# Performance work log

Measured on AMD Instinct MI355X. Metric: run time of the kernel, lower is better.

The kernel has to match this reference:

```python
import jax, jax.numpy as jnp
import numpy as np
import math

DIM_IN = 2
DIM_HIDDEN = 64
DIM_OUT = 16
NUM_LAYERS = 5  # num_layers-1 = 4 hidden SirenLayers per subnet + 1 last layer
W0 = 30.0
W0_INITIAL = 30.0
S0 = 0.0
C = 6.0
N_POINTS = 262144


def wire(w0, s0, z):
    # sin(w0*z) * exp(-(s0*z)^2)
    return jnp.sin(w0 * z) * jnp.exp(-jnp.square(s0 * z))


def setup_inputs() -> dict:
    key = jax.random.key(0)
    ks = jax.random.split(key, 8)
    # NOTE: source passes is_first=False for every layer, so init bound is
    # sqrt(c/dim_in)/layer_w0 for ALL layers (including the first).
    std0 = math.sqrt(C / DIM_IN) / W0_INITIAL
    stdh = math.sqrt(C / DIM_HIDDEN) / W0
    stdl = math.sqrt(C / DIM_HIDDEN) / W0
    u = lambda k, shape, s: jax.random.uniform(k, shape, jnp.float32, -s, s)
    nmid = NUM_LAYERS - 2  # hidden->hidden layers per subnet (3)
    return {
        "x": jax.random.uniform(ks[0], (N_POINTS, DIM_IN), jnp.float32),
        "W0m": u(ks[1], (DIM_OUT, DIM_HIDDEN, DIM_IN), std0),
        "b0": u(ks[2], (DIM_OUT, DIM_HIDDEN), std0),
        "Wm": u(ks[3], (nmid, DIM_OUT, DIM_HIDDEN, DIM_HIDDEN), stdh),
        "bm": u(ks[4], (nmid, DIM_OUT, DIM_HIDDEN), stdh),
        "Wl": u(ks[5], (DIM_OUT, DIM_HIDDEN), stdl),
        "bl": u(ks[6], (DIM_OUT,), stdl),
    }


def reference(x, W0m, b0, Wm, bm, Wl, bl):
    # First layer of each subnet (uses w0_initial): [N,D] x [O,H,D] -> [N,O,H]
    h = wire(W0_INITIAL, S0, jnp.einsum("nd,ohd->noh", x, W0m) + b0)
    # Middle hidden layers (w0), scanned over the fixed layer stack.
    def body(h, wb):
        W, b = wb
        h = wire(W0, S0, jnp.einsum("noh,ogh->nog", h, W) + b)
        return h, None
    h, _ = jax.lax.scan(body, h, (Wm, bm))
    # Last layer per subnet: dim 1 output each, is_last -> +0.5, no activation.
    out = jnp.einsum("noh,oh->no", h, Wl) + bl + 0.5  # [N, dim_out]
    return out
```

## Files before the change

### kernel.cpp

```cpp
#include <hip/hip_runtime.h>

typedef short bf16x8 __attribute__((ext_vector_type(8)));
typedef float f32x16 __attribute__((ext_vector_type(16)));

#define NBGROUPS 96
#define NTILES   8192
#define SCALE 4.7746482927568601f

union Frag  { bf16x8 v; unsigned u[4]; uint4 q; };
union AccLd { float4 f4[4]; f32x16 v; };

__device__ __forceinline__ unsigned pk_bf16(float lo, float hi) {
    unsigned r;
    asm("v_cvt_pk_bf16_f32 %0, %1, %2" : "=v"(r) : "v"(lo), "v"(hi));
    return r;
}
__device__ __forceinline__ float lo_f(unsigned w) { return __uint_as_float(w << 16); }
__device__ __forceinline__ float hi_f(unsigned w) { return __uint_as_float(w & 0xffff0000u); }

__device__ __forceinline__ float sin_rev(float z) {
    float v  = z - rintf(z);
    float v2 = v * v;
    float p  = 32.765379f;
    p = fmaf(p, v2, -74.468884f);
    p = fmaf(p, v2,  81.365064f);
    p = fmaf(p, v2, -41.331084f);
    p = fmaf(p, v2,   6.2830526f);
    return p * v;
}

__device__ __forceinline__ void init_acc(f32x16* acc, const float4* ldsBias, int Lb, int hi) {
#pragma unroll
    for (int tg = 0; tg < 2; ++tg) {
        AccLd a;
        const float4* base = &ldsBias[((Lb*2+tg)*2 + hi)*4];
#pragma unroll
        for (int q = 0; q < 4; ++q) a.f4[q] = base[q];
        acc[tg] = a.v;
    }
}

__device__ __forceinline__ void transitionHL(const f32x16* acc, Frag* Bhi, Frag* Blo) {
#pragma unroll
    for (int tg = 0; tg < 2; ++tg) {
        float sv[16];
#pragma unroll
        for (int r = 0; r < 16; ++r) sv[r] = sin_rev(acc[tg][r]);
#pragma unroll
        for (int s = 0; s < 2; ++s)
#pragma unroll
            for (int wi = 0; wi < 4; ++wi) {
                float a = sv[s*8 + 2*wi], b = sv[s*8 + 2*wi + 1];
                unsigned ph = pk_bf16(a, b);
                Bhi[tg*2+s].u[wi] = ph;
                Blo[tg*2+s].u[wi] = pk_bf16(a - lo_f(ph), b - hi_f(ph));
            }
    }
}
__device__ __forceinline__ void transitionH(const f32x16* acc, Frag* Bhi) {
#pragma unroll
    for (int tg = 0; tg < 2; ++tg) {
        float sv[16];
#pragma unroll
        for (int r = 0; r < 16; ++r) sv[r] = sin_rev(acc[tg][r]);
#pragma unroll
        for (int s = 0; s < 2; ++s)
#pragma unroll
            for (int wi = 0; wi < 4; ++wi)
                Bhi[tg*2+s].u[wi] = pk_bf16(sv[s*8 + 2*wi], sv[s*8 + 2*wi + 1]);
    }
}

__global__ __launch_bounds__(256, 3)
void siren_kernel(const float* __restrict__ x, const float* __restrict__ W0m,
                  const float* __restrict__ b0, const float* __restrict__ Wm,
                  const float* __restrict__ bm, const float* __restrict__ Wl,
                  const float* __restrict__ bl, float* __restrict__ out)
{
    __shared__ uint4  ldsAhi[3*2*4*64];
    __shared__ uint4  ldsAlo[3*2*4*64];
    __shared__ float4 ldsBias[4*2*2*4];

    const int tid  = threadIdx.x;
    const int pg   = blockIdx.x;
    const int o    = blockIdx.y;
    const int lane = tid & 63;
    const int wv   = tid >> 6;
    const int col  = lane & 31;
    const int hi   = lane >> 5;

    for (int idx = tid; idx < 3*2*4*64; idx += 256) {
        int l2  = idx & 63;
        int fi  = idx >> 6;
        int c   = fi & 3;
        int tg  = (fi >> 2) & 1;
        int L   = fi >> 3;
        int hi2 = l2 >> 5;
        int g   = tg*32 + (l2 & 31);
        int th  = c >> 1, s = c & 1;
        const float2* Wrow2 = (const float2*)(Wm + (((size_t)(L*16 + o)*64 + g)*64));
        uint4 whi, wlo;
        unsigned* uh = (unsigned*)&whi;
        unsigned* ul = (unsigned*)&wlo;
#pragma unroll
        for (int wi = 0; wi < 4; ++wi) {
            int h = th*32 + s*16 + 8*(wi>>1) + 2*(wi&1) + 4*hi2;
            float2 wp = Wrow2[h >> 1];
            float a = SCALE*wp.x, b = SCALE*wp.y;
            unsigned ph = pk_bf16(a, b);
            uh[wi] = ph;
            ul[wi] = pk_bf16(a - lo_f(ph), b - hi_f(ph));
        }
        ldsAhi[idx] = whi;
        ldsAlo[idx] = wlo;
    }
    if (tid < 64) {
        int q   = tid & 3;
        int hi2 = (tid >> 2) & 1;
        int tg  = (tid >> 3) & 1;
        int Lb  = tid >> 4;
        int h0  = tg*32 + 8*q + 4*hi2;
        const float* bsrc = (Lb < 3) ? (bm + (Lb*16 + o)*64) : (b0 + o*64);
        ldsBias[tid] = make_float4(SCALE*bsrc[h0], SCALE*bsrc[h0+1],
                                   SCALE*bsrc[h0+2], SCALE*bsrc[h0+3]);
    }

    Frag L1A[2];
#pragma unroll
    for (int tg = 0; tg < 2; ++tg) {
        int g = tg*32 + col;
        float2 wp = ((const float2*)W0m)[o*64 + g];
        float s0 = SCALE*wp.x, s1 = SCALE*wp.y;
        unsigned u0 = pk_bf16(s0, s0), u1 = pk_bf16(s1, s1);
        float l0 = s0 - lo_f(u0), l1 = s1 - lo_f(u1);
        L1A[tg].u[0] = hi ? 0u : u0;
        L1A[tg].u[1] = hi ? 0u : u1;
        L1A[tg].u[2] = hi ? 0u : pk_bf16(l0, l0);
        L1A[tg].u[3] = hi ? 0u : pk_bf16(l1, l1);
    }
    Frag WlA[4];
#pragma unroll
    for (int c = 0; c < 4; ++c) { WlA[c].u[0]=0u; WlA[c].u[1]=0u; WlA[c].u[2]=0u; WlA[c].u[3]=0u; }
    if (col == 0) {
        const float2* Wl2 = (const float2*)(Wl + o*64);
#pragma unroll
        for (int c = 0; c < 4; ++c) {
            int tg = c >> 1, s = c & 1;
#pragma unroll
            for (int wi = 0; wi < 4; ++wi) {
                int h = tg*32 + s*16 + 8*(wi>>1) + 2*(wi&1) + 4*hi;
                float2 wp = Wl2[h >> 1];
                WlA[c].u[wi] = pk_bf16(wp.x, wp.y);
            }
        }
    }
    const float blv = bl[o] + 0.5f;

    __syncthreads();

    const int tend = ((pg + 1) * NTILES) / NBGROUPS;
    for (int t = (pg * NTILES) / NBGROUPS + wv; t < tend; t += 4) {
        const int pp = t*32 + col;

        float2 xv = ((const float2*)x)[pp];
        unsigned ux = pk_bf16(xv.x, xv.y);
        float x0h = lo_f(ux), x1h = hi_f(ux);
        unsigned w0 = pk_bf16(x0h, xv.x - x0h);
        unsigned w1 = pk_bf16(x1h, xv.y - x1h);
        Frag B1;
        B1.u[0] = hi ? 0u : w0;
        B1.u[1] = hi ? 0u : w1;
        B1.u[2] = hi ? 0u : w0;
        B1.u[3] = hi ? 0u : w1;

        f32x16 acc[2];
        init_acc(acc, ldsBias, 3, hi);
        acc[0] = __builtin_amdgcn_mfma_f32_32x32x16_bf16(L1A[0].v, B1.v, acc[0], 0, 0, 0);
        acc[1] = __builtin_amdgcn_mfma_f32_32x32x16_bf16(L1A[1].v, B1.v, acc[1], 0, 0, 0);

        Frag Bhi[4], Blo[4];
        transitionHL(acc, Bhi, Blo);

#pragma unroll
        for (int L = 0; L < 3; ++L) {
            init_acc(acc, ldsBias, L, hi);
#pragma unroll
            for (int c = 0; c < 4; ++c) {
                Frag Ah0, Ah1, Al0, Al1;
                Ah0.q = ldsAhi[((L*2+0)*4+c)*64 + lane];
                Ah1.q = ldsAhi[((L*2+1)*4+c)*64 + lane];
                Al0.q = ldsAlo[((L*2+0)*4+c)*64 + lane];
                Al1.q = ldsAlo[((L*2+1)*4+c)*64 + lane];
                acc[0] = __builtin_amdgcn_mfma_f32_32x32x16_bf16(Ah0.v, Bhi[c].v, acc[0], 0, 0, 0);
                acc[1] = __builtin_amdgcn_mfma_f32_32x32x16_bf16(Ah1.v, Bhi[c].v, acc[1], 0, 0, 0);
                acc[0] = __builtin_amdgcn_mfma_f32_32x32x16_bf16(Ah0.v, Blo[c].v, acc[0], 0, 0, 0);
                acc[1] = __builtin_amdgcn_mfma_f32_32x32x16_bf16(Ah1.v, Blo[c].v, acc[1], 0, 0, 0);
                acc[0] = __builtin_amdgcn_mfma_f32_32x32x16_bf16(Al0.v, Bhi[c].v, acc[0], 0, 0, 0);
                acc[1] = __builtin_amdgcn_mfma_f32_32x32x16_bf16(Al1.v, Bhi[c].v, acc[1], 0, 0, 0);
            }
            if (L < 2) transitionHL(acc, Bhi, Blo);
        }

        transitionH(acc, Bhi);
        f32x16 facc;
#pragma unroll
        for (int i = 0; i < 16; ++i) facc[i] = 0.f;
        facc[0] = blv;
#pragma unroll
        for (int c = 0; c < 4; ++c)
            facc = __builtin_amdgcn_mfma_f32_32x32x16_bf16(WlA[c].v, Bhi[c].v, facc, 0, 0, 0);
        if (lane < 32) out[(size_t)pp*16 + o] = facc[0];
    }
}

extern "C" void kernel_launch(void* const* d_in, const int* in_sizes, int n_in,
                              void* d_out, int out_size, void* d_ws, size_t ws_size,
                              hipStream_t stream) {
    (void)in_sizes; (void)n_in; (void)out_size; (void)d_ws; (void)ws_size;
    siren_kernel<<<dim3(NBGROUPS, 16), dim3(256), 0, stream>>>(
        (const float*)d_in[0], (const float*)d_in[1], (const float*)d_in[2],
        (const float*)d_in[3], (const float*)d_in[4], (const float*)d_in[5],
        (const float*)d_in[6], (float*)d_out);
}
```

Measured before the change: 397.5 us.

## Rewrite SIREN kernel with 16x16x32 MFMA, dual tiles, packed sin, reduced split precision

The kernel is rebuilt around 16x16x32 bf16 MFMAs, with each wave processing two 16-point tiles at once so that every LDS weight fragment is reused across both. The sine polynomial is computed on packed float pairs. The last hidden layer drops its low-order bf16 correction terms, and the final linear layer becomes a VALU FMA reduction with shuffles instead of a mostly-zero MFMA. Block size goes to 512 threads with a fixed 16-iteration loop and 64 point groups. The intent is less wasted MFMA work and better weight reuse, at the cost of some accuracy in the last layer and a fixed tiling that assumes N is 262144.

```diff
diff --git a/kernel.cpp b/kernel.cpp
--- a/kernel.cpp
+++ b/kernel.cpp
@@ -1,15 +1,17 @@
 #include <hip/hip_runtime.h>
 
-typedef short bf16x8 __attribute__((ext_vector_type(8)));
-typedef float f32x16 __attribute__((ext_vector_type(16)));
-
-#define NBGROUPS 96
-#define NTILES   8192
+typedef float    f32x4 __attribute__((ext_vector_type(4)));
+typedef float    f32x2 __attribute__((ext_vector_type(2)));
+typedef unsigned u32x4 __attribute__((ext_vector_type(4)));
+
+#define NBGROUPS 64
 #define SCALE 4.7746482927568601f
 
-union Frag  { bf16x8 v; unsigned u[4]; uint4 q; };
-union AccLd { float4 f4[4]; f32x16 v; };
-
+union Frag { unsigned u[4]; u32x4 q; };
+
+__device__ __forceinline__ void mfma16(f32x4& d, u32x4 a, u32x4 b) {
+    asm("v_mfma_f32_16x16x32_bf16 %0, %1, %2, %0" : "+v"(d) : "v"(a), "v"(b));
+}
 __device__ __forceinline__ unsigned pk_bf16(float lo, float hi) {
     unsigned r;
     asm("v_cvt_pk_bf16_f32 %0, %1, %2" : "=v"(r) : "v"(lo), "v"(hi));
@@ -18,198 +20,254 @@
 __device__ __forceinline__ float lo_f(unsigned w) { return __uint_as_float(w << 16); }
 __device__ __forceinline__ float hi_f(unsigned w) { return __uint_as_float(w & 0xffff0000u); }
 
-__device__ __forceinline__ float sin_rev(float z) {
-    float v  = z - rintf(z);
-    float v2 = v * v;
-    float p  = 32.765379f;
-    p = fmaf(p, v2, -74.468884f);
-    p = fmaf(p, v2,  81.365064f);
-    p = fmaf(p, v2, -41.331084f);
-    p = fmaf(p, v2,   6.2830526f);
+__device__ __forceinline__ f32x2 sin2(f32x2 z) {
+    f32x2 r  = { rintf(z.x), rintf(z.y) };
+    f32x2 v  = z - r;
+    f32x2 v2 = v * v;
+    f32x2 p  = { 32.765379f, 32.765379f };
+    p = __builtin_elementwise_fma(p, v2, (f32x2){-74.468884f, -74.468884f});
+    p = __builtin_elementwise_fma(p, v2, (f32x2){ 81.365064f,  81.365064f});
+    p = __builtin_elementwise_fma(p, v2, (f32x2){-41.331084f, -41.331084f});
+    p = __builtin_elementwise_fma(p, v2, (f32x2){  6.2830526f,  6.2830526f});
     return p * v;
 }
 
-__device__ __forceinline__ void init_acc(f32x16* acc, const float4* ldsBias, int Lb, int hi) {
-#pragma unroll
-    for (int tg = 0; tg < 2; ++tg) {
-        AccLd a;
-        const float4* base = &ldsBias[((Lb*2+tg)*2 + hi)*4];
-#pragma unroll
-        for (int q = 0; q < 4; ++q) a.f4[q] = base[q];
-        acc[tg] = a.v;
-    }
-}
-
-__device__ __forceinline__ void transitionHL(const f32x16* acc, Frag* Bhi, Frag* Blo) {
-#pragma unroll
-    for (int tg = 0; tg < 2; ++tg) {
-        float sv[16];
-#pragma unroll
-        for (int r = 0; r < 16; ++r) sv[r] = sin_rev(acc[tg][r]);
-#pragma unroll
-        for (int s = 0; s < 2; ++s)
-#pragma unroll
-            for (int wi = 0; wi < 4; ++wi) {
-                float a = sv[s*8 + 2*wi], b = sv[s*8 + 2*wi + 1];
-                unsigned ph = pk_bf16(a, b);
-                Bhi[tg*2+s].u[wi] = ph;
-                Blo[tg*2+s].u[wi] = pk_bf16(a - lo_f(ph), b - hi_f(ph));
+__device__ __forceinline__ f32x4 bias_c(const f32x4* ldsBias, int Lb, int t, int g2) {
+    return ldsBias[(Lb*4 + t)*4 + g2];
+}
+
+__device__ __forceinline__ void transHL(const f32x4* acc, Frag* Bhi, Frag* Blo) {
+#pragma unroll
+    for (int m = 0; m < 2; ++m)
+#pragma unroll
+        for (int s = 0; s < 2; ++s) {
+            const int t = 2*m + s;
+#pragma unroll
+            for (int jp = 0; jp < 2; ++jp) {
+                f32x2 z = { acc[t][2*jp], acc[t][2*jp+1] };
+                f32x2 sv = sin2(z);
+                unsigned ph = pk_bf16(sv.x, sv.y);
+                f32x2 hf = { lo_f(ph), hi_f(ph) };
+                f32x2 d  = sv - hf;
+                Bhi[m].u[2*s+jp] = ph;
+                Blo[m].u[2*s+jp] = pk_bf16(d.x, d.y);
             }
-    }
-}
-__device__ __forceinline__ void transitionH(const f32x16* acc, Frag* Bhi) {
-#pragma unroll
-    for (int tg = 0; tg < 2; ++tg) {
-        float sv[16];
-#pragma unroll
-        for (int r = 0; r < 16; ++r) sv[r] = sin_rev(acc[tg][r]);
-#pragma unroll
-        for (int s = 0; s < 2; ++s)
-#pragma unroll
-            for (int wi = 0; wi < 4; ++wi)
-                Bhi[tg*2+s].u[wi] = pk_bf16(sv[s*8 + 2*wi], sv[s*8 + 2*wi + 1]);
-    }
-}
-
-__global__ __launch_bounds__(256, 3)
+        }
+}
+__device__ __forceinline__ void transH(const f32x4* acc, Frag* Bhi) {
+#pragma unroll
+    for (int m = 0; m < 2; ++m)
+#pragma unroll
+        for (int s = 0; s < 2; ++s) {
+            const int t = 2*m + s;
+#pragma unroll
+            for (int jp = 0; jp < 2; ++jp) {
+                f32x2 z = { acc[t][2*jp], acc[t][2*jp+1] };
+                f32x2 sv = sin2(z);
+                Bhi[m].u[2*s+jp] = pk_bf16(sv.x, sv.y);
+            }
+        }
+}
+
+__device__ __forceinline__ void layerHL(f32x4* accA, f32x4* accB,
+        const Frag* BhiA, const Frag* BloA, const Frag* BhiB, const Frag* BloB,
+        const u32x4* ldsAhi, const u32x4* ldsAlo, int L, int lane) {
+#pragma unroll
+    for (int m = 0; m < 2; ++m)
+#pragma unroll
+        for (int t = 0; t < 4; ++t) {
+            u32x4 Ah = ldsAhi[((L*4+t)*2+m)*64 + lane];
+            u32x4 Al = ldsAlo[((L*4+t)*2+m)*64 + lane];
+            mfma16(accA[t], Ah, BhiA[m].q);
+            mfma16(accB[t], Ah, BhiB[m].q);
+            mfma16(accA[t], Ah, BloA[m].q);
+            mfma16(accB[t], Ah, BloB[m].q);
+            mfma16(accA[t], Al, BhiA[m].q);
+            mfma16(accB[t], Al, BhiB[m].q);
+        }
+}
+__device__ __forceinline__ void layerH(f32x4* accA, f32x4* accB,
+        const Frag* BhiA, const Frag* BhiB,
+        const u32x4* ldsAhi, int L, int lane) {
+#pragma unroll
+    for (int m = 0; m < 2; ++m)
+#pragma unroll
+        for (int t = 0; t < 4; ++t) {
+            u32x4 Ah = ldsAhi[((L*4+t)*2+m)*64 + lane];
+            mfma16(accA[t], Ah, BhiA[m].q);
+            mfma16(accB[t], Ah, BhiB[m].q);
+        }
+}
+
+__global__ __launch_bounds__(512, 4)
 void siren_kernel(const float* __restrict__ x, const float* __restrict__ W0m,
                   const float* __restrict__ b0, const float* __restrict__ Wm,
                   const float* __restrict__ bm, const float* __restrict__ Wl,
                   const float* __restrict__ bl, float* __restrict__ out)
 {
-    __shared__ uint4  ldsAhi[3*2*4*64];
-    __shared__ uint4  ldsAlo[3*2*4*64];
-    __shared__ float4 ldsBias[4*2*2*4];
+    __shared__ u32x4 ldsAhi[3*4*2*64];
+    __shared__ u32x4 ldsAlo[2*4*2*64];
+    __shared__ f32x4 ldsBias[4*4*4];
+    __shared__ float ldsWl[4][16];
 
     const int tid  = threadIdx.x;
     const int pg   = blockIdx.x;
     const int o    = blockIdx.y;
     const int lane = tid & 63;
     const int wv   = tid >> 6;
-    const int col  = lane & 31;
-    const int hi   = lane >> 5;
-
-    for (int idx = tid; idx < 3*2*4*64; idx += 256) {
-        int l2  = idx & 63;
-        int fi  = idx >> 6;
-        int c   = fi & 3;
-        int tg  = (fi >> 2) & 1;
-        int L   = fi >> 3;
-        int hi2 = l2 >> 5;
-        int g   = tg*32 + (l2 & 31);
-        int th  = c >> 1, s = c & 1;
+    const int pl   = lane & 15;
+    const int g2   = lane >> 4;
+
+    for (int idx = tid; idx < 3*4*2*64; idx += 512) {
+        int l2 = idx & 63;
+        int fi = idx >> 6;
+        int m  = fi & 1;
+        int t  = (fi >> 1) & 3;
+        int L  = fi >> 3;
+        int g  = 16*t + (l2 & 15);
+        int gg = l2 >> 4;
         const float2* Wrow2 = (const float2*)(Wm + (((size_t)(L*16 + o)*64 + g)*64));
-        uint4 whi, wlo;
+        u32x4 whi, wlo;
         unsigned* uh = (unsigned*)&whi;
         unsigned* ul = (unsigned*)&wlo;
 #pragma unroll
-        for (int wi = 0; wi < 4; ++wi) {
-            int h = th*32 + s*16 + 8*(wi>>1) + 2*(wi&1) + 4*hi2;
-            float2 wp = Wrow2[h >> 1];
+        for (int w = 0; w < 4; ++w) {
+            int s  = w >> 1, jp = (w & 1) * 2;
+            int k  = 32*m + 16*s + 4*gg + jp;
+            float2 wp = Wrow2[k >> 1];
             float a = SCALE*wp.x, b = SCALE*wp.y;
             unsigned ph = pk_bf16(a, b);
-            uh[wi] = ph;
-            ul[wi] = pk_bf16(a - lo_f(ph), b - hi_f(ph));
+            uh[w] = ph;
+            ul[w] = pk_bf16(a - lo_f(ph), b - hi_f(ph));
         }
         ldsAhi[idx] = whi;
-        ldsAlo[idx] = wlo;
+        if (idx < 2*4*2*64) ldsAlo[idx] = wlo;
     }
     if (tid < 64) {
-        int q   = tid & 3;
-        int hi2 = (tid >> 2) & 1;
-        int tg  = (tid >> 3) & 1;
-        int Lb  = tid >> 4;
-        int h0  = tg*32 + 8*q + 4*hi2;
+        int gg = tid & 3;
+        int t  = (tid >> 2) & 3;
+        int Lb = tid >> 4;
+        int h0 = 16*t + 4*gg;
         const float* bsrc = (Lb < 3) ? (bm + (Lb*16 + o)*64) : (b0 + o*64);
-        ldsBias[tid] = make_float4(SCALE*bsrc[h0], SCALE*bsrc[h0+1],
-                                   SCALE*bsrc[h0+2], SCALE*bsrc[h0+3]);
-    }
-
-    Frag L1A[2];
-#pragma unroll
-    for (int tg = 0; tg < 2; ++tg) {
-        int g = tg*32 + col;
+        ldsBias[tid] = (f32x4){SCALE*bsrc[h0], SCALE*bsrc[h0+1],
+                               SCALE*bsrc[h0+2], SCALE*bsrc[h0+3]};
+    }
+    if (tid >= 64 && tid < 128) {
+        int t2  = tid - 64;
+        int gg  = t2 >> 4;
+        int idx = t2 & 15;
+        int t   = idx >> 2;
+        int j   = idx & 3;
+        ldsWl[gg][idx] = Wl[o*64 + 16*t + 4*gg + j];
+    }
+
+    Frag L1A[4];
+#pragma unroll
+    for (int t = 0; t < 4; ++t) {
+        int g = 16*t + pl;
         float2 wp = ((const float2*)W0m)[o*64 + g];
         float s0 = SCALE*wp.x, s1 = SCALE*wp.y;
-        unsigned u0 = pk_bf16(s0, s0), u1 = pk_bf16(s1, s1);
-        float l0 = s0 - lo_f(u0), l1 = s1 - lo_f(u1);
-        L1A[tg].u[0] = hi ? 0u : u0;
-        L1A[tg].u[1] = hi ? 0u : u1;
-        L1A[tg].u[2] = hi ? 0u : pk_bf16(l0, l0);
-        L1A[tg].u[3] = hi ? 0u : pk_bf16(l1, l1);
-    }
-    Frag WlA[4];
-#pragma unroll
-    for (int c = 0; c < 4; ++c) { WlA[c].u[0]=0u; WlA[c].u[1]=0u; WlA[c].u[2]=0u; WlA[c].u[3]=0u; }
-    if (col == 0) {
-        const float2* Wl2 = (const float2*)(Wl + o*64);
-#pragma unroll
-        for (int c = 0; c < 4; ++c) {
-            int tg = c >> 1, s = c & 1;
-#pragma unroll
-            for (int wi = 0; wi < 4; ++wi) {
-                int h = tg*32 + s*16 + 8*(wi>>1) + 2*(wi&1) + 4*hi;
-                float2 wp = Wl2[h >> 1];
-                WlA[c].u[wi] = pk_bf16(wp.x, wp.y);
+        unsigned u0 = pk_bf16(s0, s0);
+        float w0h = lo_f(u0), w0l = s0 - w0h;
+        unsigned u1 = pk_bf16(s1, s1);
+        float w1h = lo_f(u1), w1l = s1 - w1h;
+        bool zz = (g2 != 0);
+        L1A[t].u[0] = zz ? 0u : u0;
+        L1A[t].u[1] = zz ? 0u : pk_bf16(w0l, w1h);
+        L1A[t].u[2] = zz ? 0u : pk_bf16(w1h, w1l);
+        L1A[t].u[3] = 0u;
+    }
+    const float blv = bl[o] + 0.5f;
+
+    __syncthreads();
+
+#pragma unroll 1
+    for (int it = 0; it < 16; ++it) {
+        const int t32 = pg*128 + it*8 + wv;
+        const int pb  = t32*32;
+
+        float2 xa = ((const float2*)x)[pb + pl];
+        float2 xb = ((const float2*)x)[pb + 16 + pl];
+        Frag B1a, B1b;
+        {
+            unsigned u0 = pk_bf16(xa.x, xa.x);
+            float x0h = lo_f(u0), x0l = xa.x - x0h;
+            unsigned u1 = pk_bf16(xa.y, xa.y);
+            float x1h = lo_f(u1), x1l = xa.y - x1h;
+            B1a.u[0] = pk_bf16(x0h, x0l);
+            B1a.u[1] = pk_bf16(x0h, x1h);
+            B1a.u[2] = pk_bf16(x1l, x1h);
+            B1a.u[3] = 0u;
+            u0 = pk_bf16(xb.x, xb.x); x0h = lo_f(u0); x0l = xb.x - x0h;
+            u1 = pk_bf16(xb.y, xb.y); x1h = lo_f(u1); x1l = xb.y - x1h;
+            B1b.u[0] = pk_bf16(x0h, x0l);
+            B1b.u[1] = pk_bf16(x0h, x1h);
+            B1b.u[2] = pk_bf16(x1l, x1h);
+            B1b.u[3] = 0u;
+        }
+
+        f32x4 accA[4], accB[4];
+#pragma unroll
+        for (int t = 0; t < 4; ++t) {
+            accA[t] = bias_c(ldsBias, 3, t, g2);
+            accB[t] = bias_c(ldsBias, 3, t, g2);
+        }
+#pragma unroll
+        for (int t = 0; t < 4; ++t) mfma16(accA[t], L1A[t].q, B1a.q);
+#pragma unroll
+        for (int t = 0; t < 4; ++t) mfma16(accB[t], L1A[t].q, B1b.q);
+
+        Frag BhiA[2], BloA[2], BhiB[2], BloB[2];
+        transHL(accA, BhiA, BloA);
+        transHL(accB, BhiB, BloB);
+
+#pragma unroll
+        for (int t = 0; t < 4; ++t) {
+            accA[t] = bias_c(ldsBias, 0, t, g2);
+            accB[t] = bias_c(ldsBias, 0, t, g2);
+        }
+        layerHL(accA, accB, BhiA, BloA, BhiB, BloB, ldsAhi, ldsAlo, 0, lane);
+        transHL(accA, BhiA, BloA);
+        transHL(accB, BhiB, BloB);
+
+#pragma unroll
+        for (int t = 0; t < 4; ++t) {
+            accA[t] = bias_c(ldsBias, 1, t, g2);
+            accB[t] = bias_c(ldsBias, 1, t, g2);
+        }
+        layerHL(accA, accB, BhiA, BloA, BhiB, BloB, ldsAhi, ldsAlo, 1, lane);
+        transH(accA, BhiA);
+        transH(accB, BhiB);
+
+#pragma unroll
+        for (int t = 0; t < 4; ++t) {
+            accA[t] = bias_c(ldsBias, 2, t, g2);
+            accB[t] = bias_c(ldsBias, 2, t, g2);
+        }
+        layerH(accA, accB, BhiA, BhiB, ldsAhi, 2, lane);
+
+        const f32x2* wl2 = (const f32x2*)&ldsWl[g2][0];
+        f32x2 sa = {0.f, 0.f}, sb = {0.f, 0.f};
+#pragma unroll
+        for (int t = 0; t < 4; ++t)
+#pragma unroll
+            for (int jp = 0; jp < 2; ++jp) {
+                f32x2 w = wl2[t*2 + jp];
+                f32x2 za = { accA[t][2*jp], accA[t][2*jp+1] };
+                f32x2 zb = { accB[t][2*jp], accB[t][2*jp+1] };
+                sa = __builtin_elementwise_fma(sin2(za), w, sa);
+                sb = __builtin_elementwise_fma(sin2(zb), w, sb);
             }
-        }
-    }
-    const float blv = bl[o] + 0.5f;
-
-    __syncthreads();
-
-    const int tend = ((pg + 1) * NTILES) / NBGROUPS;
-    for (int t = (pg * NTILES) / NBGROUPS + wv; t < tend; t += 4) {
-        const int pp = t*32 + col;
-
-        float2 xv = ((const float2*)x)[pp];
-        unsigned ux = pk_bf16(xv.x, xv.y);
-        float x0h = lo_f(ux), x1h = hi_f(ux);
-        unsigned w0 = pk_bf16(x0h, xv.x - x0h);
-        unsigned w1 = pk_bf16(x1h, xv.y - x1h);
-        Frag B1;
-        B1.u[0] = hi ? 0u : w0;
-        B1.u[1] = hi ? 0u : w1;
-        B1.u[2] = hi ? 0u : w0;
-        B1.u[3] = hi ? 0u : w1;
-
-        f32x16 acc[2];
-        init_acc(acc, ldsBias, 3, hi);
-        acc[0] = __builtin_amdgcn_mfma_f32_32x32x16_bf16(L1A[0].v, B1.v, acc[0], 0, 0, 0);
-        acc[1] = __builtin_amdgcn_mfma_f32_32x32x16_bf16(L1A[1].v, B1.v, acc[1], 0, 0, 0);
-
-        Frag Bhi[4], Blo[4];
-        transitionHL(acc, Bhi, Blo);
-
-#pragma unroll
-        for (int L = 0; L < 3; ++L) {
-            init_acc(acc, ldsBias, L, hi);
-#pragma unroll
-            for (int c = 0; c < 4; ++c) {
-                Frag Ah0, Ah1, Al0, Al1;
-                Ah0.q = ldsAhi[((L*2+0)*4+c)*64 + lane];
-                Ah1.q = ldsAhi[((L*2+1)*4+c)*64 + lane];
-                Al0.q = ldsAlo[((L*2+0)*4+c)*64 + lane];
-                Al1.q = ldsAlo[((L*2+1)*4+c)*64 + lane];
-                acc[0] = __builtin_amdgcn_mfma_f32_32x32x16_bf16(Ah0.v, Bhi[c].v, acc[0], 0, 0, 0);
-                acc[1] = __builtin_amdgcn_mfma_f32_32x32x16_bf16(Ah1.v, Bhi[c].v, acc[1], 0, 0, 0);
-                acc[0] = __builtin_amdgcn_mfma_f32_32x32x16_bf16(Ah0.v, Blo[c].v, acc[0], 0, 0, 0);
-                acc[1] = __builtin_amdgcn_mfma_f32_32x32x16_bf16(Ah1.v, Blo[c].v, acc[1], 0, 0, 0);
-                acc[0] = __builtin_amdgcn_mfma_f32_32x32x16_bf16(Al0.v, Bhi[c].v, acc[0], 0, 0, 0);
-                acc[1] = __builtin_amdgcn_mfma_f32_32x32x16_bf16(Al1.v, Bhi[c].v, acc[1], 0, 0, 0);
-            }
-            if (L < 2) transitionHL(acc, Bhi, Blo);
-        }
-
-        transitionH(acc, Bhi);
-        f32x16 facc;
-#pragma unroll
-        for (int i = 0; i < 16; ++i) facc[i] = 0.f;
-        facc[0] = blv;
-#pragma unroll
-        for (int c = 0; c < 4; ++c)
-            facc = __builtin_amdgcn_mfma_f32_32x32x16_bf16(WlA[c].v, Bhi[c].v, facc, 0, 0, 0);
-        if (lane < 32) out[(size_t)pp*16 + o] = facc[0];
+        float suma = sa.x + sa.y;
+        float sumb = sb.x + sb.y;
+        suma += __shfl_xor(suma, 16);
+        suma += __shfl_xor(suma, 32);
+        sumb += __shfl_xor(sumb, 16);
+        sumb += __shfl_xor(sumb, 32);
+        if (lane < 32) {
+            float v = (lane < 16 ? suma : sumb) + blv;
+            out[(size_t)(pb + lane)*16 + o] = v;
+        }
     }
 }
 
@@ -217,7 +275,7 @@
                               void* d_out, int out_size, void* d_ws, size_t ws_size,
                               hipStream_t stream) {
     (void)in_sizes; (void)n_in; (void)out_size; (void)d_ws; (void)ws_size;
-    siren_kernel<<<dim3(NBGROUPS, 16), dim3(256), 0, stream>>>(
+    siren_kernel<<<dim3(NBGROUPS, 16), dim3(512), 0, stream>>>(
         (const float*)d_in[0], (const float*)d_in[1], (const float*)d_in[2],
         (const float*)d_in[3], (const float*)d_in[4], (const float*)d_in[5],
         (const float*)d_in[6], (float*)d_out);
```

Measured after the change: 354.6 us. -10.8%, faster.
